# Kernel tuning notes

Hardware: AMD Instinct MI355X
Metric: run time of the kernel (lower is better)

The kernel has to match this reference:

```python
import jax, jax.numpy as jnp
import numpy as np

ALPHA = 0.5  # leak/integration rate of the EI cell

B, L, D = 512, 64, 784
N_EXC, N_INH, N_CLS = 128, 32, 10


def setup_inputs() -> dict:
    key = jax.random.key(0)
    ks = jax.random.split(key, 11)
    s_in = 1.0 / np.sqrt(D)
    s_e = 1.0 / np.sqrt(N_EXC)
    s_i = 1.0 / np.sqrt(N_INH)
    return {
        "x_seq": jax.random.normal(ks[0], (B, L, D), jnp.float32),
        "Wxe": jax.random.normal(ks[1], (N_EXC, D), jnp.float32) * s_in,
        "Wxi": jax.random.normal(ks[2], (N_INH, D), jnp.float32) * s_in,
        "Wee": jax.random.normal(ks[3], (N_EXC, N_EXC), jnp.float32) * s_e,
        "Wie": jax.random.normal(ks[4], (N_EXC, N_INH), jnp.float32) * s_i,
        "Wei": jax.random.normal(ks[5], (N_INH, N_EXC), jnp.float32) * s_e,
        "Wii": jax.random.normal(ks[6], (N_INH, N_INH), jnp.float32) * s_i,
        "be": jax.random.normal(ks[7], (N_EXC,), jnp.float32) * 0.01,
        "bi": jax.random.normal(ks[8], (N_INH,), jnp.float32) * 0.01,
        "W_ro": jax.random.normal(ks[9], (N_CLS, N_EXC), jnp.float32) * s_e,
        "b_ro": jax.random.normal(ks[10], (N_CLS,), jnp.float32) * 0.01,
    }


def reference(x_seq, Wxe, Wxi, Wee, Wie, Wei, Wii, be, bi, W_ro, b_ro):
    # Dale's law: rectify weight magnitudes so exc/inh signs are structural.
    Wxe_p, Wxi_p = jax.nn.relu(Wxe), jax.nn.relu(Wxi)
    Wee_p, Wie_p = jax.nn.relu(Wee), jax.nn.relu(Wie)
    Wei_p, Wii_p = jax.nn.relu(Wei), jax.nn.relu(Wii)

    def step(carry, x_t):  # x_t: [B, D]
        e, i = carry
        r_e = jax.nn.relu(e)
        r_i = jax.nn.relu(i)
        exc_e = x_t @ Wxe_p.T + r_e @ Wee_p.T          # [B, n_exc]
        inh_e = r_i @ Wie_p.T                           # [B, n_exc]
        exc_i = x_t @ Wxi_p.T + r_e @ Wei_p.T           # [B, n_inh]
        inh_i = r_i @ Wii_p.T                           # [B, n_inh]
        e_new = (1.0 - ALPHA) * e + ALPHA * (exc_e - inh_e + be)
        i_new = (1.0 - ALPHA) * i + ALPHA * (exc_i - inh_i + bi)
        r_e_new = jax.nn.relu(e_new)
        r_i_new = jax.nn.relu(i_new)
        bal_e = exc_e - inh_e
        bal_i = exc_i - inh_i
        logits_t = r_e_new @ W_ro.T + b_ro              # readout(F.relu(e))
        return (e_new, i_new), (logits_t, r_e_new, r_i_new, bal_e, bal_i)

    Bn = x_seq.shape[0]
    e0 = jnp.zeros((Bn, Wee.shape[0]), x_seq.dtype)
    i0 = jnp.zeros((Bn, Wii.shape[0]), x_seq.dtype)
    _, outs = jax.lax.scan(step, (e0, i0), jnp.swapaxes(x_seq, 0, 1))  # time-major
    logits_seq, r_e_seq, r_i_seq, bal_e_seq, bal_i_seq = (
        jnp.swapaxes(o, 0, 1) for o in outs)  # back to [B, L, ...]
    return logits_seq, logits_seq[:, -1, :], r_e_seq, r_i_seq, bal_e_seq, bal_i_seq
```

## Files before the change

### kernel.cpp

```cpp
#include <hip/hip_runtime.h>

#define NE 128
#define NI 32
#define NT 160
#define NC 10
#define BB 512
#define LL 64
#define DD 784
#define KP 800
#define MM (BB*LL)

#define G_OFF   0
#define G_SZ    (NT*NT)
#define WH_OFF  (G_OFF + G_SZ)
#define WL_OFF  (WH_OFF + 64000)
#define U_OFF   (WL_OFF + 64000)
#define U_SZ    (MM*NT)

#define O_LOGITS 0
#define O_LAST   327680
#define O_RE     332800
#define O_RI     4527104
#define O_BALE   5575680
#define O_BALI   9769984

#define LDS_BARRIER() asm volatile("s_waitcnt lgkmcnt(0)\n\ts_barrier" ::: "memory")

typedef __attribute__((ext_vector_type(8))) short short8;
typedef __attribute__((ext_vector_type(4))) float af4;

static __device__ __forceinline__ unsigned short f2bf(float f) {
  unsigned u = __float_as_uint(f);
  return (unsigned short)((u + 0x7FFFu + ((u >> 16) & 1u)) >> 16);
}
static __device__ __forceinline__ float bf2f(unsigned short h) {
  return __uint_as_float((unsigned)h << 16);
}

static __device__ __forceinline__ void cvt_split8(const float* f, short8& ah, short8& al) {
  union { short8 s; unsigned u[4]; } H, L;
  #pragma unroll
  for (int p = 0; p < 4; ++p) {
    float lo = f[2*p], hi = f[2*p+1];
    unsigned h;
    asm("v_cvt_pk_bf16_f32 %0, %1, %2" : "=v"(h) : "v"(lo), "v"(hi));
    float rl = lo - __uint_as_float(h << 16);
    float rh = hi - __uint_as_float(h & 0xffff0000u);
    unsigned l;
    asm("v_cvt_pk_bf16_f32 %0, %1, %2" : "=v"(l) : "v"(rl), "v"(rh));
    H.u[p] = h; L.u[p] = l;
  }
  ah = H.s; al = L.s;
}

__global__ void prep_kernel(const float* __restrict__ Wxe, const float* __restrict__ Wxi,
                            const float* __restrict__ Wee, const float* __restrict__ Wie,
                            const float* __restrict__ Wei, const float* __restrict__ Wii,
                            float* __restrict__ ws) {
  int idx = blockIdx.x * blockDim.x + threadIdx.x;
  const int total = G_SZ + NT * KP;
  if (idx >= total) return;
  if (idx < G_SZ) {
    int k = idx / NT, j = idx % NT;
    float g;
    if (j < NE) {
      if (k < NE) g =  fmaxf(Wee[j*NE + k], 0.f);
      else        g = -fmaxf(Wie[j*NI + (k-NE)], 0.f);
    } else {
      int ji = j - NE;
      if (k < NE) g =  fmaxf(Wei[ji*NE + k], 0.f);
      else        g = -fmaxf(Wii[ji*NI + (k-NE)], 0.f);
    }
    ws[G_OFF + k*NT + j] = g;
  } else {
    int t = idx - G_SZ;
    int n = t / KP, k = t - n * KP;
    float v = 0.f;
    if (k < DD)
      v = (n < NE) ? fmaxf(Wxe[n*DD + k], 0.f) : fmaxf(Wxi[(n-NE)*DD + k], 0.f);
    unsigned short h = f2bf(v);
    unsigned short l = f2bf(v - bf2f(h));
    ((unsigned short*)(ws + WH_OFF))[t] = h;
    ((unsigned short*)(ws + WL_OFF))[t] = l;
  }
}

static __device__ __forceinline__ void stage_tile(const unsigned short* __restrict__ Wh,
                                                  const unsigned short* __restrict__ Wl,
                                                  unsigned short* dstBase, int kb, int tid) {
  #pragma unroll
  for (int i = 0; i < 5; ++i) {
    const int idx = i * 256 + tid;
    const int row = idx >> 3;
    const int phys = idx & 7;
    const int logical = phys ^ (row & 7);
    const unsigned short* src =
        ((logical & 4) ? Wl : Wh) + (size_t)row * KP + kb + (logical & 3) * 8;
    __builtin_amdgcn_global_load_lds(
        (const __attribute__((address_space(1))) unsigned int*)src,
        (__attribute__((address_space(3))) unsigned int*)(dstBase + idx * 8),
        16, 0, 0);
  }
}

__global__ __launch_bounds__(256, 1) void gemm_kernel(const float* __restrict__ X,
                                                      const float* __restrict__ ws,
                                                      float* __restrict__ U) {
  __shared__ unsigned short tile[2][10240];

  const int tid  = threadIdx.x;
  const int lane = tid & 63;
  const int wave = tid >> 6;
  const int n16  = lane & 15;
  const int quad = lane >> 4;
  const int sw   = n16 & 7;
  const int mbase = blockIdx.x * 128 + wave * 32;

  const unsigned short* Wh = (const unsigned short*)(ws + WH_OFF);
  const unsigned short* Wl = (const unsigned short*)(ws + WL_OFF);

  af4 acc[2][10];
  #pragma unroll
  for (int ms = 0; ms < 2; ++ms)
    #pragma unroll
    for (int nt = 0; nt < 10; ++nt)
      #pragma unroll
      for (int r = 0; r < 4; ++r) acc[ms][nt][r] = 0.f;

  const float* xr0 = X + (size_t)(mbase + n16) * DD;
  const float* xr1 = xr0 + (size_t)16 * DD;

  stage_tile(Wh, Wl, tile[0], 0, tid);
  float fa0[8], fa1[8];
  {
    const int kb = quad * 8;
    float4 v0 = *(const float4*)(xr0 + kb);
    float4 v1 = *(const float4*)(xr0 + kb + 4);
    fa0[0]=v0.x; fa0[1]=v0.y; fa0[2]=v0.z; fa0[3]=v0.w;
    fa0[4]=v1.x; fa0[5]=v1.y; fa0[6]=v1.z; fa0[7]=v1.w;
    float4 w0 = *(const float4*)(xr1 + kb);
    float4 w1 = *(const float4*)(xr1 + kb + 4);
    fa1[0]=w0.x; fa1[1]=w0.y; fa1[2]=w0.z; fa1[3]=w0.w;
    fa1[4]=w1.x; fa1[5]=w1.y; fa1[6]=w1.z; fa1[7]=w1.w;
  }
  __syncthreads();

  for (int ks = 0; ks < 25; ++ks) {
    const int cur = ks & 1;
    if (ks < 24) stage_tile(Wh, Wl, tile[cur ^ 1], (ks + 1) * 32, tid);

    float nf0[8] = {0,0,0,0,0,0,0,0};
    float nf1[8] = {0,0,0,0,0,0,0,0};
    {
      const int nkb = (ks + 1) * 32 + quad * 8;
      if (nkb < DD) {
        float4 v0 = *(const float4*)(xr0 + nkb);
        float4 v1 = *(const float4*)(xr0 + nkb + 4);
        nf0[0]=v0.x; nf0[1]=v0.y; nf0[2]=v0.z; nf0[3]=v0.w;
        nf0[4]=v1.x; nf0[5]=v1.y; nf0[6]=v1.z; nf0[7]=v1.w;
        float4 w0 = *(const float4*)(xr1 + nkb);
        float4 w1 = *(const float4*)(xr1 + nkb + 4);
        nf1[0]=w0.x; nf1[1]=w0.y; nf1[2]=w0.z; nf1[3]=w0.w;
        nf1[4]=w1.x; nf1[5]=w1.y; nf1[6]=w1.z; nf1[7]=w1.w;
      }
    }

    short8 bh[10], bl[10];
    const unsigned short* tb = tile[cur];
    #pragma unroll
    for (int nt = 0; nt < 10; ++nt) {
      const int ro = (nt * 16 + n16) * 64;
      bh[nt] = *(const short8*)(tb + ro + ((quad ^ sw) << 3));
      bl[nt] = *(const short8*)(tb + ro + (((4 | quad) ^ sw) << 3));
    }

    short8 ah0, al0, ah1, al1;
    cvt_split8(fa0, ah0, al0);
    cvt_split8(fa1, ah1, al1);

    #pragma unroll
    for (int nt = 0; nt < 10; ++nt) {
      acc[0][nt] = __builtin_amdgcn_mfma_f32_16x16x32_bf16(ah0, bh[nt], acc[0][nt], 0, 0, 0);
      acc[1][nt] = __builtin_amdgcn_mfma_f32_16x16x32_bf16(ah1, bh[nt], acc[1][nt], 0, 0, 0);
      acc[0][nt] = __builtin_amdgcn_mfma_f32_16x16x32_bf16(ah0, bl[nt], acc[0][nt], 0, 0, 0);
      acc[1][nt] = __builtin_amdgcn_mfma_f32_16x16x32_bf16(ah1, bl[nt], acc[1][nt], 0, 0, 0);
      acc[0][nt] = __builtin_amdgcn_mfma_f32_16x16x32_bf16(al0, bh[nt], acc[0][nt], 0, 0, 0);
      acc[1][nt] = __builtin_amdgcn_mfma_f32_16x16x32_bf16(al1, bh[nt], acc[1][nt], 0, 0, 0);
    }

    #pragma unroll
    for (int j = 0; j < 8; ++j) { fa0[j] = nf0[j]; fa1[j] = nf1[j]; }

    __syncthreads();
  }

  #pragma unroll
  for (int ms = 0; ms < 2; ++ms)
    #pragma unroll
    for (int nt = 0; nt < 10; ++nt)
      #pragma unroll
      for (int r = 0; r < 4; ++r) {
        const int row = mbase + ms * 16 + quad * 4 + r;
        U[(size_t)row * NT + nt * 16 + n16] = acc[ms][nt][r];
      }
}

__global__ __launch_bounds__(256, 2) void recur_kernel(
    const float* __restrict__ ws,
    const float* __restrict__ be, const float* __restrict__ bi,
    float* __restrict__ out) {
  __shared__ float rbuf[2][NT];
  __shared__ float balbuf[2][NT];
  __shared__ float biasL[NT];

  const int tid  = threadIdx.x;
  const int lane = tid & 63;
  const int wave = tid >> 6;
  const int jc   = (wave << 3) | (lane & 7);
  const int kc   = (lane >> 3) & 7;
  const int j0   = jc * 5;
  const int k0   = kc * 20;
  const int b    = blockIdx.x;

  const float* G = ws + G_OFF;
  const float* U = ws + U_OFF;

  float g[20][5];
  #pragma unroll
  for (int kk = 0; kk < 20; ++kk)
    #pragma unroll
    for (int c = 0; c < 5; ++c)
      g[kk][c] = G[(size_t)(k0 + kk) * NT + j0 + c];

  if (tid < NT) biasL[tid] = (tid < NE) ? be[tid] : bi[tid - NE];
  for (int i = tid; i < 2 * NT; i += 256) (&rbuf[0][0])[i] = 0.f;

  const bool owner = (kc == 0);
  float u[5];
  if (owner) {
    const size_t ub = ((size_t)b * LL) * NT + j0;
    #pragma unroll
    for (int c = 0; c < 5; ++c) u[c] = U[ub + c];
  }
  float s[5];
  #pragma unroll
  for (int c = 0; c < 5; ++c) s[c] = 0.f;

  __syncthreads();

  for (int l = 0; l < LL; ++l) {
    const int p = l & 1;
    if (l > 0) {
      const size_t ob = (size_t)b * LL + (l - 1);
      if (tid < NE) {
        out[O_RE   + ob * NE + tid] = rbuf[p][tid];
        out[O_BALE + ob * NE + tid] = balbuf[p][tid];
      } else if (tid < NT) {
        const int j2 = tid - NE;
        out[O_RI   + ob * NI + j2] = rbuf[p][NE + j2];
        out[O_BALI + ob * NI + j2] = balbuf[p][NE + j2];
      }
    }
    float nu[5];
    if (owner && l + 1 < LL) {
      const size_t nb = ((size_t)b * LL + (l + 1)) * NT + j0;
      #pragma unroll
      for (int c = 0; c < 5; ++c) nu[c] = U[nb + c];
    }
    float a[5];
    #pragma unroll
    for (int c = 0; c < 5; ++c) a[c] = 0.f;
    #pragma unroll
    for (int kk4 = 0; kk4 < 5; ++kk4) {
      float4 rv = *(const float4*)(&rbuf[p][k0 + kk4 * 4]);
      #pragma unroll
      for (int c = 0; c < 5; ++c)
        a[c] += rv.x * g[kk4*4+0][c] + rv.y * g[kk4*4+1][c]
              + rv.z * g[kk4*4+2][c] + rv.w * g[kk4*4+3][c];
    }
    #pragma unroll
    for (int c = 0; c < 5; ++c) {
      float v = a[c];
      v += __shfl_xor(v, 8, 64);
      v += __shfl_xor(v, 16, 64);
      v += __shfl_xor(v, 32, 64);
      a[c] = v;
    }
    if (owner) {
      #pragma unroll
      for (int c = 0; c < 5; ++c) {
        float bal = a[c] + u[c];
        balbuf[1 - p][j0 + c] = bal;
        float sn = 0.5f * (s[c] + bal + biasL[j0 + c]);
        s[c] = sn;
        rbuf[1 - p][j0 + c] = fmaxf(sn, 0.f);
      }
      #pragma unroll
      for (int c = 0; c < 5; ++c) u[c] = nu[c];
    }
    LDS_BARRIER();
  }
  {
    const size_t ob = (size_t)b * LL + 63;
    if (tid < NE) {
      out[O_RE   + ob * NE + tid] = rbuf[0][tid];
      out[O_BALE + ob * NE + tid] = balbuf[0][tid];
    } else if (tid < NT) {
      const int j2 = tid - NE;
      out[O_RI   + ob * NI + j2] = rbuf[0][NE + j2];
      out[O_BALI + ob * NI + j2] = balbuf[0][NE + j2];
    }
  }
}

__global__ __launch_bounds__(256) void logits_kernel(const float* __restrict__ Wro,
                                                     const float* __restrict__ bro,
                                                     float* __restrict__ out) {
  __shared__ unsigned short BH[16][136];
  __shared__ unsigned short BL[16][136];
  __shared__ float broL[16];

  const int tid  = threadIdx.x;
  const int lane = tid & 63;
  const int wave = tid >> 6;
  const int n16  = lane & 15;
  const int quad = lane >> 4;

  for (int i = tid; i < 16 * NE; i += 256) {
    const int n = i >> 7, k = i & 127;
    float v = (n < NC) ? Wro[n * NE + k] : 0.f;
    unsigned short h = f2bf(v);
    BH[n][k] = h;
    BL[n][k] = f2bf(v - bf2f(h));
  }
  if (tid < 16) broL[tid] = (tid < NC) ? bro[tid] : 0.f;
  __syncthreads();

  const int mbase = blockIdx.x * 128 + wave * 32;
  const float* re = out + O_RE;

  af4 acc[2];
  #pragma unroll
  for (int ms = 0; ms < 2; ++ms)
    #pragma unroll
    for (int r = 0; r < 4; ++r) acc[ms][r] = broL[n16];

  short8 ah[2][4], al[2][4];
  #pragma unroll
  for (int ms = 0; ms < 2; ++ms) {
    const float* row = re + (size_t)(mbase + ms * 16 + n16) * NE;
    #pragma unroll
    for (int kf = 0; kf < 4; ++kf) {
      const int kb = kf * 32 + quad * 8;
      float4 v0 = *(const float4*)(row + kb);
      float4 v1 = *(const float4*)(row + kb + 4);
      float f[8] = {v0.x, v0.y, v0.z, v0.w, v1.x, v1.y, v1.z, v1.w};
      cvt_split8(f, ah[ms][kf], al[ms][kf]);
    }
  }
  short8 bh[4], bl[4];
  #pragma unroll
  for (int kf = 0; kf < 4; ++kf) {
    const int kb = kf * 32 + quad * 8;
    bh[kf] = *(const short8*)(&BH[n16][kb]);
    bl[kf] = *(const short8*)(&BL[n16][kb]);
  }
  #pragma unroll
  for (int kf = 0; kf < 4; ++kf)
    #pragma unroll
    for (int ms = 0; ms < 2; ++ms) {
      acc[ms] = __builtin_amdgcn_mfma_f32_16x16x32_bf16(ah[ms][kf], bh[kf], acc[ms], 0, 0, 0);
      acc[ms] = __builtin_amdgcn_mfma_f32_16x16x32_bf16(ah[ms][kf], bl[kf], acc[ms], 0, 0, 0);
      acc[ms] = __builtin_amdgcn_mfma_f32_16x16x32_bf16(al[ms][kf], bh[kf], acc[ms], 0, 0, 0);
    }

  if (n16 < NC) {
    #pragma unroll
    for (int ms = 0; ms < 2; ++ms)
      #pragma unroll
      for (int r = 0; r < 4; ++r) {
        const int m = mbase + ms * 16 + quad * 4 + r;
        out[O_LOGITS + (size_t)m * NC + n16] = acc[ms][r];
        if ((m & 63) == 63)
          out[O_LAST + (size_t)(m >> 6) * NC + n16] = acc[ms][r];
      }
  }
}

extern "C" void kernel_launch(void* const* d_in, const int* in_sizes, int n_in,
                              void* d_out, int out_size, void* d_ws, size_t ws_size,
                              hipStream_t stream) {
  const float* x   = (const float*)d_in[0];
  const float* Wxe = (const float*)d_in[1];
  const float* Wxi = (const float*)d_in[2];
  const float* Wee = (const float*)d_in[3];
  const float* Wie = (const float*)d_in[4];
  const float* Wei = (const float*)d_in[5];
  const float* Wii = (const float*)d_in[6];
  const float* be  = (const float*)d_in[7];
  const float* bi  = (const float*)d_in[8];
  const float* Wro = (const float*)d_in[9];
  const float* bro = (const float*)d_in[10];
  float* ws  = (float*)d_ws;
  float* out = (float*)d_out;

  hipLaunchKernelGGL(prep_kernel, dim3((G_SZ + NT*KP + 255)/256), dim3(256), 0, stream,
                     Wxe, Wxi, Wee, Wie, Wei, Wii, ws);
  hipLaunchKernelGGL(gemm_kernel, dim3(MM/128), dim3(256), 0, stream,
                     x, ws, ws + U_OFF);
  hipLaunchKernelGGL(recur_kernel, dim3(BB), dim3(256), 0, stream,
                     ws, be, bi, out);
  hipLaunchKernelGGL(logits_kernel, dim3(MM/128), dim3(256), 0, stream,
                     Wro, bro, out);
}
```

Baseline: 275.4 us.

## Process two batch rows per recurrence block with shared-memory recurrent matrix

```diff
diff --git a/kernel.cpp b/kernel.cpp
--- a/kernel.cpp
+++ b/kernel.cpp
@@ -205,110 +205,116 @@
       }
 }
 
-__global__ __launch_bounds__(256, 2) void recur_kernel(
+__global__ __launch_bounds__(512, 1) void recur_kernel(
     const float* __restrict__ ws,
     const float* __restrict__ be, const float* __restrict__ bi,
     float* __restrict__ out) {
-  __shared__ float rbuf[2][NT];
-  __shared__ float balbuf[2][NT];
+  extern __shared__ float Gs[];
+  __shared__ float rbuf[2][2][NT];
+  __shared__ float balbuf[2][2][NT];
+  __shared__ float pbuf[4][2][NT];
   __shared__ float biasL[NT];
 
   const int tid  = threadIdx.x;
   const int lane = tid & 63;
   const int wave = tid >> 6;
-  const int jc   = (wave << 3) | (lane & 7);
-  const int kc   = (lane >> 3) & 7;
+  const int jc   = (lane & 15) | ((wave & 1) << 4);
+  const int kc   = (lane >> 4) | ((wave >> 1) << 2);
+  const int half = wave >> 1;
   const int j0   = jc * 5;
-  const int k0   = kc * 20;
-  const int b    = blockIdx.x;
+  const int k0   = kc * 10;
+  const int b0   = blockIdx.x * 2;
 
   const float* G = ws + G_OFF;
   const float* U = ws + U_OFF;
 
-  float g[20][5];
-  #pragma unroll
-  for (int kk = 0; kk < 20; ++kk)
-    #pragma unroll
-    for (int c = 0; c < 5; ++c)
-      g[kk][c] = G[(size_t)(k0 + kk) * NT + j0 + c];
+  for (int i = tid; i < G_SZ / 4; i += 512)
+    ((float4*)Gs)[i] = ((const float4*)G)[i];
 
   if (tid < NT) biasL[tid] = (tid < NE) ? be[tid] : bi[tid - NE];
-  for (int i = tid; i < 2 * NT; i += 256) (&rbuf[0][0])[i] = 0.f;
-
-  const bool owner = (kc == 0);
-  float u[5];
+  for (int i = tid; i < 2 * 2 * NT; i += 512) (&rbuf[0][0][0])[i] = 0.f;
+
+  const bool owner = tid < NT;
+  float u0 = 0.f, u1 = 0.f, s0 = 0.f, s1 = 0.f;
   if (owner) {
-    const size_t ub = ((size_t)b * LL) * NT + j0;
-    #pragma unroll
-    for (int c = 0; c < 5; ++c) u[c] = U[ub + c];
-  }
-  float s[5];
-  #pragma unroll
-  for (int c = 0; c < 5; ++c) s[c] = 0.f;
-
+    u0 = U[((size_t)b0 * LL) * NT + tid];
+    u1 = U[((size_t)(b0 + 1) * LL) * NT + tid];
+  }
   __syncthreads();
 
   for (int l = 0; l < LL; ++l) {
     const int p = l & 1;
-    if (l > 0) {
-      const size_t ob = (size_t)b * LL + (l - 1);
-      if (tid < NE) {
-        out[O_RE   + ob * NE + tid] = rbuf[p][tid];
-        out[O_BALE + ob * NE + tid] = balbuf[p][tid];
-      } else if (tid < NT) {
-        const int j2 = tid - NE;
-        out[O_RI   + ob * NI + j2] = rbuf[p][NE + j2];
-        out[O_BALI + ob * NI + j2] = balbuf[p][NE + j2];
-      }
-    }
-    float nu[5];
+    if (l > 0 && tid < 2 * NT) {
+      const int r = tid / NT, j = tid % NT;
+      const size_t ob = (size_t)(b0 + r) * LL + (l - 1);
+      if (j < NE) {
+        out[O_RE   + ob * NE + j] = rbuf[p][r][j];
+        out[O_BALE + ob * NE + j] = balbuf[p][r][j];
+      } else {
+        out[O_RI   + ob * NI + (j - NE)] = rbuf[p][r][j];
+        out[O_BALI + ob * NI + (j - NE)] = balbuf[p][r][j];
+      }
+    }
+    float nu0 = 0.f, nu1 = 0.f;
     if (owner && l + 1 < LL) {
-      const size_t nb = ((size_t)b * LL + (l + 1)) * NT + j0;
-      #pragma unroll
-      for (int c = 0; c < 5; ++c) nu[c] = U[nb + c];
-    }
-    float a[5];
-    #pragma unroll
-    for (int c = 0; c < 5; ++c) a[c] = 0.f;
-    #pragma unroll
-    for (int kk4 = 0; kk4 < 5; ++kk4) {
-      float4 rv = *(const float4*)(&rbuf[p][k0 + kk4 * 4]);
-      #pragma unroll
-      for (int c = 0; c < 5; ++c)
-        a[c] += rv.x * g[kk4*4+0][c] + rv.y * g[kk4*4+1][c]
-              + rv.z * g[kk4*4+2][c] + rv.w * g[kk4*4+3][c];
-    }
-    #pragma unroll
-    for (int c = 0; c < 5; ++c) {
-      float v = a[c];
-      v += __shfl_xor(v, 8, 64);
-      v += __shfl_xor(v, 16, 64);
-      v += __shfl_xor(v, 32, 64);
-      a[c] = v;
-    }
-    if (owner) {
+      nu0 = U[((size_t)b0 * LL + l + 1) * NT + tid];
+      nu1 = U[((size_t)(b0 + 1) * LL + l + 1) * NT + tid];
+    }
+    float a0[5], a1[5];
+    #pragma unroll
+    for (int c = 0; c < 5; ++c) { a0[c] = 0.f; a1[c] = 0.f; }
+    #pragma unroll
+    for (int kk2 = 0; kk2 < 5; ++kk2) {
+      float2 r0 = *(const float2*)(&rbuf[p][0][k0 + kk2 * 2]);
+      float2 r1 = *(const float2*)(&rbuf[p][1][k0 + kk2 * 2]);
+      const float* g0 = &Gs[(k0 + kk2 * 2) * NT + j0];
+      const float* g1 = g0 + NT;
       #pragma unroll
       for (int c = 0; c < 5; ++c) {
-        float bal = a[c] + u[c];
-        balbuf[1 - p][j0 + c] = bal;
-        float sn = 0.5f * (s[c] + bal + biasL[j0 + c]);
-        s[c] = sn;
-        rbuf[1 - p][j0 + c] = fmaxf(sn, 0.f);
-      }
+        float ga = g0[c], gb = g1[c];
+        a0[c] += r0.x * ga + r0.y * gb;
+        a1[c] += r1.x * ga + r1.y * gb;
+      }
+    }
+    #pragma unroll
+    for (int c = 0; c < 5; ++c) {
+      float v0 = a0[c], v1 = a1[c];
+      v0 += __shfl_xor(v0, 16, 64);  v1 += __shfl_xor(v1, 16, 64);
+      v0 += __shfl_xor(v0, 32, 64);  v1 += __shfl_xor(v1, 32, 64);
+      a0[c] = v0; a1[c] = v1;
+    }
+    if ((lane >> 4) == 0) {
       #pragma unroll
-      for (int c = 0; c < 5; ++c) u[c] = nu[c];
+      for (int c = 0; c < 5; ++c) {
+        pbuf[half][0][j0 + c] = a0[c];
+        pbuf[half][1][j0 + c] = a1[c];
+      }
     }
     LDS_BARRIER();
-  }
-  {
-    const size_t ob = (size_t)b * LL + 63;
-    if (tid < NE) {
-      out[O_RE   + ob * NE + tid] = rbuf[0][tid];
-      out[O_BALE + ob * NE + tid] = balbuf[0][tid];
-    } else if (tid < NT) {
-      const int j2 = tid - NE;
-      out[O_RI   + ob * NI + j2] = rbuf[0][NE + j2];
-      out[O_BALI + ob * NI + j2] = balbuf[0][NE + j2];
+    if (owner) {
+      const int j = tid;
+      float bal0 = pbuf[0][0][j] + pbuf[1][0][j] + pbuf[2][0][j] + pbuf[3][0][j] + u0;
+      float bal1 = pbuf[0][1][j] + pbuf[1][1][j] + pbuf[2][1][j] + pbuf[3][1][j] + u1;
+      balbuf[1 - p][0][j] = bal0;
+      balbuf[1 - p][1][j] = bal1;
+      float sn0 = 0.5f * (s0 + bal0 + biasL[j]);
+      float sn1 = 0.5f * (s1 + bal1 + biasL[j]);
+      s0 = sn0; s1 = sn1;
+      rbuf[1 - p][0][j] = fmaxf(sn0, 0.f);
+      rbuf[1 - p][1][j] = fmaxf(sn1, 0.f);
+      u0 = nu0; u1 = nu1;
+    }
+    LDS_BARRIER();
+  }
+  if (tid < 2 * NT) {
+    const int r = tid / NT, j = tid % NT;
+    const size_t ob = (size_t)(b0 + r) * LL + 63;
+    if (j < NE) {
+      out[O_RE   + ob * NE + j] = rbuf[0][r][j];
+      out[O_BALE + ob * NE + j] = balbuf[0][r][j];
+    } else {
+      out[O_RI   + ob * NI + (j - NE)] = rbuf[0][r][j];
+      out[O_BALI + ob * NI + (j - NE)] = balbuf[0][r][j];
     }
   }
 }
@@ -408,7 +414,7 @@
                      Wxe, Wxi, Wee, Wie, Wei, Wii, ws);
   hipLaunchKernelGGL(gemm_kernel, dim3(MM/128), dim3(256), 0, stream,
                      x, ws, ws + U_OFF);
-  hipLaunchKernelGGL(recur_kernel, dim3(BB), dim3(256), 0, stream,
+  hipLaunchKernelGGL(recur_kernel, dim3(BB/2), dim3(512), G_SZ * sizeof(float), stream,
                      ws, be, bi, out);
   hipLaunchKernelGGL(logits_kernel, dim3(MM/128), dim3(256), 0, stream,
                      Wro, bro, out);
```

New measurement: 313.2 us. 1.14x slower.

## Batch four sequences per recurrence block and stream tiled weights from cache

Applied to the files above, without the earlier changes.

```diff
diff --git a/kernel.cpp b/kernel.cpp
--- a/kernel.cpp
+++ b/kernel.cpp
@@ -71,7 +71,8 @@
       if (k < NE) g =  fmaxf(Wei[ji*NE + k], 0.f);
       else        g = -fmaxf(Wii[ji*NI + (k-NE)], 0.f);
     }
-    ws[G_OFF + k*NT + j] = g;
+    const int dst = ((k / 20) * 32 + (j / 5)) * 100 + (k % 20) * 5 + (j % 5);
+    ws[G_OFF + dst] = g;
   } else {
     int t = idx - G_SZ;
     int n = t / KP, k = t - n * KP;
@@ -205,12 +206,12 @@
       }
 }
 
-__global__ __launch_bounds__(256, 2) void recur_kernel(
+__global__ __launch_bounds__(256, 1) void recur_kernel(
     const float* __restrict__ ws,
     const float* __restrict__ be, const float* __restrict__ bi,
     float* __restrict__ out) {
-  __shared__ float rbuf[2][NT];
-  __shared__ float balbuf[2][NT];
+  __shared__ float rbuf[2][4][NT];
+  __shared__ float balbuf[2][4][NT];
   __shared__ float biasL[NT];
 
   const int tid  = threadIdx.x;
@@ -220,95 +221,119 @@
   const int kc   = (lane >> 3) & 7;
   const int j0   = jc * 5;
   const int k0   = kc * 20;
-  const int b    = blockIdx.x;
-
-  const float* G = ws + G_OFF;
-  const float* U = ws + U_OFF;
-
-  float g[20][5];
-  #pragma unroll
-  for (int kk = 0; kk < 20; ++kk)
-    #pragma unroll
-    for (int c = 0; c < 5; ++c)
-      g[kk][c] = G[(size_t)(k0 + kk) * NT + j0 + c];
+  const int b0   = blockIdx.x * 4;
+
+  const float* Gp = ws + G_OFF + (kc * 32 + jc) * 100;
+  const float* U  = ws + U_OFF;
 
   if (tid < NT) biasL[tid] = (tid < NE) ? be[tid] : bi[tid - NE];
-  for (int i = tid; i < 2 * NT; i += 256) (&rbuf[0][0])[i] = 0.f;
+  for (int i = tid; i < 2 * 4 * NT; i += 256) (&rbuf[0][0][0])[i] = 0.f;
 
   const bool owner = (kc == 0);
-  float u[5];
+  float u[4][5], s[4][5];
+  #pragma unroll
+  for (int r = 0; r < 4; ++r)
+    #pragma unroll
+    for (int c = 0; c < 5; ++c) { u[r][c] = 0.f; s[r][c] = 0.f; }
   if (owner) {
-    const size_t ub = ((size_t)b * LL) * NT + j0;
-    #pragma unroll
-    for (int c = 0; c < 5; ++c) u[c] = U[ub + c];
-  }
-  float s[5];
-  #pragma unroll
-  for (int c = 0; c < 5; ++c) s[c] = 0.f;
-
+    #pragma unroll
+    for (int r = 0; r < 4; ++r) {
+      const size_t ub = ((size_t)(b0 + r) * LL) * NT + j0;
+      #pragma unroll
+      for (int c = 0; c < 5; ++c) u[r][c] = U[ub + c];
+    }
+  }
   __syncthreads();
 
   for (int l = 0; l < LL; ++l) {
     const int p = l & 1;
     if (l > 0) {
-      const size_t ob = (size_t)b * LL + (l - 1);
-      if (tid < NE) {
-        out[O_RE   + ob * NE + tid] = rbuf[p][tid];
-        out[O_BALE + ob * NE + tid] = balbuf[p][tid];
-      } else if (tid < NT) {
-        const int j2 = tid - NE;
-        out[O_RI   + ob * NI + j2] = rbuf[p][NE + j2];
-        out[O_BALI + ob * NI + j2] = balbuf[p][NE + j2];
-      }
-    }
-    float nu[5];
+      #pragma unroll
+      for (int r = 0; r < 4; ++r) {
+        const size_t ob = (size_t)(b0 + r) * LL + (l - 1);
+        if (tid < NE) {
+          out[O_RE   + ob * NE + tid] = rbuf[p][r][tid];
+          out[O_BALE + ob * NE + tid] = balbuf[p][r][tid];
+        } else if (tid < NT) {
+          const int j2 = tid - NE;
+          out[O_RI   + ob * NI + j2] = rbuf[p][r][NE + j2];
+          out[O_BALI + ob * NI + j2] = balbuf[p][r][NE + j2];
+        }
+      }
+    }
+    float nu[4][5];
+    #pragma unroll
+    for (int r = 0; r < 4; ++r)
+      #pragma unroll
+      for (int c = 0; c < 5; ++c) nu[r][c] = 0.f;
     if (owner && l + 1 < LL) {
-      const size_t nb = ((size_t)b * LL + (l + 1)) * NT + j0;
-      #pragma unroll
-      for (int c = 0; c < 5; ++c) nu[c] = U[nb + c];
-    }
-    float a[5];
-    #pragma unroll
-    for (int c = 0; c < 5; ++c) a[c] = 0.f;
-    #pragma unroll
-    for (int kk4 = 0; kk4 < 5; ++kk4) {
-      float4 rv = *(const float4*)(&rbuf[p][k0 + kk4 * 4]);
-      #pragma unroll
-      for (int c = 0; c < 5; ++c)
-        a[c] += rv.x * g[kk4*4+0][c] + rv.y * g[kk4*4+1][c]
-              + rv.z * g[kk4*4+2][c] + rv.w * g[kk4*4+3][c];
-    }
-    #pragma unroll
-    for (int c = 0; c < 5; ++c) {
-      float v = a[c];
-      v += __shfl_xor(v, 8, 64);
-      v += __shfl_xor(v, 16, 64);
-      v += __shfl_xor(v, 32, 64);
-      a[c] = v;
-    }
+      #pragma unroll
+      for (int r = 0; r < 4; ++r) {
+        const size_t nb = ((size_t)(b0 + r) * LL + (l + 1)) * NT + j0;
+        #pragma unroll
+        for (int c = 0; c < 5; ++c) nu[r][c] = U[nb + c];
+      }
+    }
+    float rr[4][20];
+    #pragma unroll
+    for (int r = 0; r < 4; ++r)
+      #pragma unroll
+      for (int q = 0; q < 5; ++q) {
+        float4 v = *(const float4*)(&rbuf[p][r][k0 + q * 4]);
+        rr[r][q*4+0] = v.x; rr[r][q*4+1] = v.y;
+        rr[r][q*4+2] = v.z; rr[r][q*4+3] = v.w;
+      }
+    float a[4][5];
+    #pragma unroll
+    for (int r = 0; r < 4; ++r)
+      #pragma unroll
+      for (int c = 0; c < 5; ++c) a[r][c] = 0.f;
+    #pragma unroll
+    for (int f = 0; f < 25; ++f) {
+      float4 gv = *(const float4*)(Gp + f * 4);
+      const float ge[4] = {gv.x, gv.y, gv.z, gv.w};
+      #pragma unroll
+      for (int i = 0; i < 4; ++i) {
+        const int t = f * 4 + i, kk = t / 5, c = t % 5;
+        #pragma unroll
+        for (int r = 0; r < 4; ++r) a[r][c] += rr[r][kk] * ge[i];
+      }
+    }
+    #pragma unroll
+    for (int r = 0; r < 4; ++r)
+      #pragma unroll
+      for (int c = 0; c < 5; ++c) {
+        float v = a[r][c];
+        v += __shfl_xor(v, 8, 64);
+        v += __shfl_xor(v, 16, 64);
+        v += __shfl_xor(v, 32, 64);
+        a[r][c] = v;
+      }
     if (owner) {
       #pragma unroll
-      for (int c = 0; c < 5; ++c) {
-        float bal = a[c] + u[c];
-        balbuf[1 - p][j0 + c] = bal;
-        float sn = 0.5f * (s[c] + bal + biasL[j0 + c]);
-        s[c] = sn;
-        rbuf[1 - p][j0 + c] = fmaxf(sn, 0.f);
-      }
-      #pragma unroll
-      for (int c = 0; c < 5; ++c) u[c] = nu[c];
+      for (int r = 0; r < 4; ++r)
+        #pragma unroll
+        for (int c = 0; c < 5; ++c) {
+          float bal = a[r][c] + u[r][c];
+          balbuf[1 - p][r][j0 + c] = bal;
+          float sn = 0.5f * (s[r][c] + bal + biasL[j0 + c]);
+          s[r][c] = sn;
+          rbuf[1 - p][r][j0 + c] = fmaxf(sn, 0.f);
+          u[r][c] = nu[r][c];
+        }
     }
     LDS_BARRIER();
   }
-  {
-    const size_t ob = (size_t)b * LL + 63;
+  #pragma unroll
+  for (int r = 0; r < 4; ++r) {
+    const size_t ob = (size_t)(b0 + r) * LL + 63;
     if (tid < NE) {
-      out[O_RE   + ob * NE + tid] = rbuf[0][tid];
-      out[O_BALE + ob * NE + tid] = balbuf[0][tid];
+      out[O_RE   + ob * NE + tid] = rbuf[0][r][tid];
+      out[O_BALE + ob * NE + tid] = balbuf[0][r][tid];
     } else if (tid < NT) {
       const int j2 = tid - NE;
-      out[O_RI   + ob * NI + j2] = rbuf[0][NE + j2];
-      out[O_BALI + ob * NI + j2] = balbuf[0][NE + j2];
+      out[O_RI   + ob * NI + j2] = rbuf[0][r][NE + j2];
+      out[O_BALI + ob * NI + j2] = balbuf[0][r][NE + j2];
     }
   }
 }
@@ -408,7 +433,7 @@
                      Wxe, Wxi, Wee, Wie, Wei, Wii, ws);
   hipLaunchKernelGGL(gemm_kernel, dim3(MM/128), dim3(256), 0, stream,
                      x, ws, ws + U_OFF);
-  hipLaunchKernelGGL(recur_kernel, dim3(BB), dim3(256), 0, stream,
+  hipLaunchKernelGGL(recur_kernel, dim3(BB/4), dim3(256), 0, stream,
                      ws, be, bi, out);
   hipLaunchKernelGGL(logits_kernel, dim3(MM/128), dim3(256), 0, stream,
                      Wro, bro, out);
```

New measurement: 409.9 us. 48.8% more time.
